# Kernel optimization log

Hardware: AMD Instinct MI355X
Metric: run time of the kernel (lower is better)

## Reference

```python
import math
import jax, jax.numpy as jnp
import numpy as np

LOG2PI = math.log(2.0 * math.pi)
B, T, N, C, K = 16, 12, 325, 64, 8
L = N * T  # 3900, Conv1d in_channels (in_features)


def _l2norm(x, axis):
    # F.normalize(x, dim=axis, p=2) with eps=1e-12
    return x / jnp.maximum(jnp.linalg.norm(x, axis=axis, keepdims=True), 1e-12)


def setup_inputs() -> dict:
    key = jax.random.key(0)
    ks = jax.random.split(key, 5)
    rep = jax.random.normal(ks[0], (B, T, N, C), jnp.float32)
    rep_aug = jax.random.normal(ks[1], (B, T, N, C), jnp.float32)
    # xavier-uniform-scale Linear weight [K, C*N*T]
    W_gamma = jax.random.normal(ks[2], (K, C * N * T), jnp.float32) * 0.005
    # Conv1d(kernel_size=1) weights [K, L]
    W_mu = jax.random.normal(ks[3], (K, L), jnp.float32) * 0.02
    b_mu = jnp.zeros((K,), jnp.float32)
    W_sigma = jax.random.normal(ks[4], (K, L), jnp.float32) * 0.01
    b_sigma = jnp.zeros((K,), jnp.float32)
    return dict(rep=rep, rep_aug=rep_aug, W_gamma=W_gamma, W_mu=W_mu,
                b_mu=b_mu, W_sigma=W_sigma, b_sigma=b_sigma)


def reference(rep, rep_aug, W_gamma, W_mu, b_mu, W_sigma, b_sigma):
    # rep: [b,t,n,c] -> [b,c,n,t]
    rep = jnp.transpose(rep, (0, 3, 2, 1))
    rep_aug = jnp.transpose(rep_aug, (0, 3, 2, 1))
    b, c = rep.shape[0], rep.shape[1]
    rep = _l2norm(rep, 1)
    rep_aug = _l2norm(rep_aug, 1)

    # gammas: softmax(Linear(flat)), [b,k]
    gam = jax.nn.softmax(rep_aug.reshape(b, -1) @ W_gamma.T, axis=-1)

    # Conv1d(kernel=1) on [b, L, c]: out[b,k,j] = sum_l W[k,l]*x[b,l,j] + bias[k]
    xa = jnp.transpose(rep_aug, (0, 2, 3, 1)).reshape(b, -1, c)  # [b,L,c]
    mus = jnp.einsum('kl,blc->bck', W_mu, xa) + b_mu              # [b,c,k]
    sigmas = jnp.exp(jnp.einsum('kl,blc->bck', W_sigma, xa) + b_sigma)

    # log pdf over broadcast [b,c,L,k]
    h = rep.reshape(b, c, -1)                                     # [b,c,L]
    z = (h[:, :, :, None] - mus[:, :, None, :]) / sigmas[:, :, None, :]
    logp = -jnp.log(sigmas)[:, :, None, :] - 0.5 * LOG2PI - 0.5 * z * z

    # prod over channel dim c, then l2norm over L (dim=1 of [b,L,k])
    comp = _l2norm(jnp.prod(logp, axis=1), 1)                     # [b,L,k]
    log_prob = comp + jnp.log(gam)[:, None, :]                    # [b,L,k]
    loss = -jnp.mean(jnp.log(jnp.sum(jnp.exp(log_prob), axis=-1)))
    return loss
```

## Files before the change

### kernel.cpp

```cpp
#include <hip/hip_runtime.h>
#include <hip/hip_bf16.h>
#include <math.h>

#define B_ 16
#define T_ 12
#define N_ 325
#define C_ 64
#define K_ 8
#define L_ 3900
#define M_ 249600
#define M4_ 62400
#define LCH_ 61
#define LOG2PI_ 1.8378770664093453f

#define OFF_LOGGAM 0
#define OFF_PART   128
#define OFF_MUS    384
#define OFF_ISIG   8576
#define OFF_T1     16768
#define OFF_SPART  24960
#define OFF_P      32768
#define OFF_AAUG   531968
#define OFF_GPART  4525568
#define OFF_CONVP  4650368

__global__ __launch_bounds__(256) void kA(const float* __restrict__ rep_aug,
                                          const float* __restrict__ Wmu,
                                          const float* __restrict__ Wsg,
                                          float* __restrict__ Aaug,
                                          float* __restrict__ convp) {
    int b = blockIdx.x / LCH_, lc = blockIdx.x - b * LCH_;
    int l0 = lc * 64;
    __shared__ float ldsA[64 * 65];
    __shared__ float sc[64];
    __shared__ float ldsW[16 * 64];
    int tid = threadIdx.x, lane = tid & 63, wv = tid >> 6;
    const float4* r4 = (const float4*)rep_aug;
    for (int i4 = tid; i4 < 1024; i4 += 256) {
        int ll = i4 >> 4, c4 = i4 & 15;
        int l = l0 + ll;
        float4 v = make_float4(0.f, 0.f, 0.f, 0.f);
        if (l < L_) {
            int n = l / T_, t = l - n * T_;
            v = r4[(size_t)((b * T_ + t) * N_ + n) * 16 + c4];
        }
        int base = ll * 65 + c4 * 4;
        ldsA[base] = v.x; ldsA[base+1] = v.y; ldsA[base+2] = v.z; ldsA[base+3] = v.w;
    }
    for (int idx = tid; idx < 1024; idx += 256) {
        int r = idx >> 6, ll = idx & 63;
        int l = l0 + ll;
        float w = 0.0f;
        if (l < L_) w = (r < 8) ? Wmu[r * L_ + l] : Wsg[(r - 8) * L_ + l];
        ldsW[r * 64 + ll] = w;
    }
    __syncthreads();
    #pragma unroll 4
    for (int i = 0; i < 16; ++i) {
        int p = wv * 16 + i;
        float x = ldsA[p * 65 + lane];
        float ss = x * x;
        #pragma unroll
        for (int m = 1; m < 64; m <<= 1) ss += __shfl_xor(ss, m);
        if (lane == 0) sc[p] = 1.0f / fmaxf(sqrtf(ss), 1e-12f);
    }
    __syncthreads();
    for (int idx = tid; idx < 4096; idx += 256) {
        int c = idx >> 6, ll = idx & 63;
        int l = l0 + ll;
        if (l < L_)
            Aaug[(size_t)(b * C_ + c) * L_ + l] = ldsA[ll * 65 + c] * sc[ll];
    }
    int c = lane, kk = wv;
    const float* w0 = &ldsW[(kk * 4 + 0) * 64];
    const float* w1 = &ldsW[(kk * 4 + 1) * 64];
    const float* w2 = &ldsW[(kk * 4 + 2) * 64];
    const float* w3 = &ldsW[(kk * 4 + 3) * 64];
    float a0 = 0.f, a1 = 0.f, a2 = 0.f, a3 = 0.f;
    #pragma unroll 8
    for (int l = 0; l < 64; ++l) {
        float a = ldsA[l * 65 + c] * sc[l];
        a0 = fmaf(a, w0[l], a0);
        a1 = fmaf(a, w1[l], a1);
        a2 = fmaf(a, w2[l], a2);
        a3 = fmaf(a, w3[l], a3);
    }
    float* dst = convp + (size_t)lc * 16384 + b * 1024 + c * 16 + kk * 4;
    dst[0] = a0; dst[1] = a1; dst[2] = a2; dst[3] = a3;
}

__global__ __launch_bounds__(256) void kB(const float* __restrict__ Aaug,
                                          const float* __restrict__ Wg,
                                          const float* __restrict__ convp,
                                          const float* __restrict__ bmu,
                                          const float* __restrict__ bsg,
                                          float* __restrict__ gpartT,
                                          float* __restrict__ mus,
                                          float* __restrict__ isig,
                                          float* __restrict__ t1) {
    int tid = threadIdx.x, lane = tid & 63, wv = tid >> 6;
    if (blockIdx.x < 975) {
        const float4* A4 = (const float4*)Aaug;
        const float4* W4 = (const float4*)Wg;
        int m4 = blockIdx.x * 64 + lane;
        float4 w[K_];
        #pragma unroll
        for (int k = 0; k < K_; ++k) w[k] = W4[(size_t)k * M4_ + m4];
        float acc[4][K_];
        #pragma unroll
        for (int bb = 0; bb < 4; ++bb) {
            float4 a = A4[(size_t)(wv * 4 + bb) * M4_ + m4];
            #pragma unroll
            for (int k = 0; k < K_; ++k)
                acc[bb][k] = a.x * w[k].x + a.y * w[k].y + a.z * w[k].z + a.w * w[k].w;
        }
        __shared__ float red[128];
        #pragma unroll
        for (int bb = 0; bb < 4; ++bb)
            #pragma unroll
            for (int k = 0; k < K_; ++k) {
                float v = acc[bb][k];
                #pragma unroll
                for (int m = 1; m < 64; m <<= 1) v += __shfl_xor(v, m);
                if (lane == 0) red[wv * 32 + bb * 8 + k] = v;
            }
        __syncthreads();
        if (tid < 128) gpartT[(size_t)tid * 975 + blockIdx.x] = red[tid];
    } else {
        int o = (blockIdx.x - 975) * 256 + tid;
        float s = 0.0f;
        #pragma unroll 8
        for (int lc = 0; lc < LCH_; ++lc) s += convp[(size_t)lc * 16384 + o];
        int bc = o >> 4, kk = o & 15, k = kk & 7;
        if (kk < 8) {
            mus[bc * 8 + k] = s + bmu[k];
        } else {
            float logit = s + bsg[k];
            isig[bc * 8 + k] = expf(-logit);
            t1[bc * 8 + k] = -logit - 0.5f * LOG2PI_;
        }
    }
}

__global__ __launch_bounds__(256) void kC(const float* __restrict__ rep,
                                          const float* __restrict__ gpartT,
                                          const float* __restrict__ mus,
                                          const float* __restrict__ isig,
                                          const float* __restrict__ t1,
                                          float* __restrict__ loggam,
                                          float* __restrict__ P,
                                          float* __restrict__ Spart) {
    int tid = threadIdx.x, lane = tid & 63, wv = tid >> 6;
    if (blockIdx.x < 16) {
        int b = blockIdx.x;
        int k = tid >> 5, i5 = tid & 31;
        float s = 0.0f;
        for (int i = i5; i < 975; i += 32) s += gpartT[(size_t)(b * 8 + k) * 975 + i];
        #pragma unroll
        for (int m = 1; m < 32; m <<= 1) s += __shfl_xor(s, m);
        __shared__ float red[8];
        if (i5 == 0) red[k] = s;
        __syncthreads();
        if (tid < 8) {
            float mx = -1e30f;
            #pragma unroll
            for (int j = 0; j < 8; ++j) mx = fmaxf(mx, red[j]);
            float sum = 0.0f;
            #pragma unroll
            for (int j = 0; j < 8; ++j) sum += expf(red[j] - mx);
            loggam[b * 8 + tid] = red[tid] - mx - logf(sum);
        }
    } else {
        int j = blockIdx.x - 16;
        int b = j / LCH_, lc = j - b * LCH_;
        int l0 = lc * 64;
        __shared__ float ldsA[64 * 65];
        __shared__ float sc[64];
        __shared__ float ldsMu[512], ldsIs[512], ldsT1[512];
        const float4* r4 = (const float4*)rep;
        for (int i4 = tid; i4 < 1024; i4 += 256) {
            int ll = i4 >> 4, c4 = i4 & 15;
            int l = l0 + ll;
            float4 v = make_float4(0.f, 0.f, 0.f, 0.f);
            if (l < L_) {
                int n = l / T_, t = l - n * T_;
                v = r4[(size_t)((b * T_ + t) * N_ + n) * 16 + c4];
            }
            int base = ll * 65 + c4 * 4;
            ldsA[base] = v.x; ldsA[base+1] = v.y; ldsA[base+2] = v.z; ldsA[base+3] = v.w;
        }
        for (int idx = tid; idx < 512; idx += 256) {
            ldsMu[idx] = mus[b * 512 + idx];
            ldsIs[idx] = isig[b * 512 + idx];
            ldsT1[idx] = t1[b * 512 + idx];
        }
        __syncthreads();
        #pragma unroll 4
        for (int i = 0; i < 16; ++i) {
            int p = wv * 16 + i;
            float x = ldsA[p * 65 + lane];
            float ss = x * x;
            #pragma unroll
            for (int m = 1; m < 64; m <<= 1) ss += __shfl_xor(ss, m);
            if (lane == 0) sc[p] = 1.0f / fmaxf(sqrtf(ss), 1e-12f);
        }
        __syncthreads();
        int l = l0 + lane;
        bool valid = l < L_;
        int k0 = wv * 2, k1 = k0 + 1;
        float scv = sc[lane];
        float p0 = 1.0f, p1 = 1.0f;
        #pragma unroll 8
        for (int c = 0; c < 64; ++c) {
            float a = ldsA[lane * 65 + c] * scv;
            float z0 = (a - ldsMu[c * 8 + k0]) * ldsIs[c * 8 + k0];
            p0 *= ldsT1[c * 8 + k0] - 0.5f * z0 * z0;
            float z1 = (a - ldsMu[c * 8 + k1]) * ldsIs[c * 8 + k1];
            p1 *= ldsT1[c * 8 + k1] - 0.5f * z1 * z1;
        }
        if (!valid) { p0 = 0.0f; p1 = 0.0f; }
        if (valid) {
            P[(size_t)(b * K_ + k0) * L_ + l] = p0;
            P[(size_t)(b * K_ + k1) * L_ + l] = p1;
        }
        float v0 = p0 * p0, v1 = p1 * p1;
        #pragma unroll
        for (int m = 1; m < 64; m <<= 1) { v0 += __shfl_xor(v0, m); v1 += __shfl_xor(v1, m); }
        if (lane == 0) {
            Spart[(size_t)(b * K_ + k0) * LCH_ + lc] = v0;
            Spart[(size_t)(b * K_ + k1) * LCH_ + lc] = v1;
        }
    }
}

__global__ __launch_bounds__(256) void kD(const float* __restrict__ P,
                                          const float* __restrict__ Spart,
                                          const float* __restrict__ loggam,
                                          float* __restrict__ part) {
    int b = blockIdx.x >> 4, ch = blockIdx.x & 15;
    int tid = threadIdx.x, lane = tid & 63, wv = tid >> 6;
    __shared__ float invk[8], lgk[8];
    if (tid < 8) {
        float s = 0.0f;
        #pragma unroll 8
        for (int i = 0; i < LCH_; ++i) s += Spart[(size_t)(b * 8 + tid) * LCH_ + i];
        invk[tid] = 1.0f / fmaxf(sqrtf(s), 1e-12f);
        lgk[tid] = loggam[b * 8 + tid];
    }
    __syncthreads();
    int l = ch * 256 + tid;
    float ll = 0.0f;
    if (l < L_) {
        float v[K_];
        float mx = -1e30f;
        #pragma unroll
        for (int k = 0; k < K_; ++k) {
            v[k] = P[(size_t)(b * K_ + k) * L_ + l] * invk[k] + lgk[k];
            mx = fmaxf(mx, v[k]);
        }
        float s = 0.0f;
        #pragma unroll
        for (int k = 0; k < K_; ++k) s += expf(v[k] - mx);
        ll = mx + logf(s);
    }
    #pragma unroll
    for (int m = 1; m < 64; m <<= 1) ll += __shfl_xor(ll, m);
    __shared__ float red[4];
    if (lane == 0) red[wv] = ll;
    __syncthreads();
    if (tid == 0) part[blockIdx.x] = red[0] + red[1] + red[2] + red[3];
}

__global__ void kE(const float* __restrict__ part, float* __restrict__ out) {
    double v = (double)part[threadIdx.x];
    #pragma unroll
    for (int m = 1; m < 64; m <<= 1) v += __shfl_xor(v, m);
    __shared__ double red[4];
    int lane = threadIdx.x & 63, wave = threadIdx.x >> 6;
    if (lane == 0) red[wave] = v;
    __syncthreads();
    if (threadIdx.x == 0)
        out[0] = (float)(-(red[0] + red[1] + red[2] + red[3]) / ((double)B_ * (double)L_));
}

extern "C" void kernel_launch(void* const* d_in, const int* in_sizes, int n_in,
                              void* d_out, int out_size, void* d_ws, size_t ws_size,
                              hipStream_t stream) {
    const float* rep     = (const float*)d_in[0];
    const float* rep_aug = (const float*)d_in[1];
    const float* Wg      = (const float*)d_in[2];
    const float* Wmu     = (const float*)d_in[3];
    const float* bmu     = (const float*)d_in[4];
    const float* Wsg     = (const float*)d_in[5];
    const float* bsg     = (const float*)d_in[6];
    float* out = (float*)d_out;
    float* ws  = (float*)d_ws;

    float* loggam = ws + OFF_LOGGAM;
    float* part   = ws + OFF_PART;
    float* mus    = ws + OFF_MUS;
    float* isig   = ws + OFF_ISIG;
    float* t1     = ws + OFF_T1;
    float* Spart  = ws + OFF_SPART;
    float* P      = ws + OFF_P;
    float* Aaug   = ws + OFF_AAUG;
    float* gpartT = ws + OFF_GPART;
    float* convp  = ws + OFF_CONVP;

    kA<<<B_ * LCH_, 256, 0, stream>>>(rep_aug, Wmu, Wsg, Aaug, convp);
    kB<<<975 + 64, 256, 0, stream>>>(Aaug, Wg, convp, bmu, bsg, gpartT, mus, isig, t1);
    kC<<<16 + B_ * LCH_, 256, 0, stream>>>(rep, gpartT, mus, isig, t1, loggam, P, Spart);
    kD<<<B_ * 16, 256, 0, stream>>>(P, Spart, loggam, part);
    kE<<<1, 256, 0, stream>>>(part, out);
}
```

Measured before the change: 59.72 us.

## Fuse gamma linear into normalization kernel and fold final reduction via atomic counter

The gamma projection (Linear over C*N*T) is now computed inside kA from the normalized rep_aug tile held in LDS. This removes the intermediate Aaug write (about 16 MB) and its reread in kB. Gamma partials per (chunk, batch) are reduced and soft-maxed in a small tail of kB, and the final scalar reduction of kE is merged into kD with a last-block atomic counter, which drops one launch. Block indexing is reordered so batch varies fastest, letting blocks with the same l-chunk share Wg and W loads. The trade-off is that each kA thread now streams Wg rows strided by L, adding global traffic and latency to kA.

```diff
diff --git a/kernel.cpp b/kernel.cpp
--- a/kernel.cpp
+++ b/kernel.cpp
@@ -1,5 +1,4 @@
 #include <hip/hip_runtime.h>
-#include <hip/hip_bf16.h>
 #include <math.h>
 
 #define B_ 16
@@ -9,27 +8,27 @@
 #define K_ 8
 #define L_ 3900
 #define M_ 249600
-#define M4_ 62400
 #define LCH_ 61
 #define LOG2PI_ 1.8378770664093453f
 
 #define OFF_LOGGAM 0
 #define OFF_PART   128
-#define OFF_MUS    384
-#define OFF_ISIG   8576
-#define OFF_T1     16768
-#define OFF_SPART  24960
-#define OFF_P      32768
-#define OFF_AAUG   531968
-#define OFF_GPART  4525568
-#define OFF_CONVP  4650368
+#define OFF_CTR    384
+#define OFF_MUS    512
+#define OFF_ISIG   8704
+#define OFF_T1     16896
+#define OFF_SPART  25088
+#define OFF_GPART  32896
+#define OFF_P      40704
+#define OFF_CONVP  539904
 
 __global__ __launch_bounds__(256) void kA(const float* __restrict__ rep_aug,
+                                          const float* __restrict__ Wg,
                                           const float* __restrict__ Wmu,
                                           const float* __restrict__ Wsg,
-                                          float* __restrict__ Aaug,
+                                          float* __restrict__ gpart,
                                           float* __restrict__ convp) {
-    int b = blockIdx.x / LCH_, lc = blockIdx.x - b * LCH_;
+    int b = blockIdx.x & 15, lc = blockIdx.x >> 4;
     int l0 = lc * 64;
     __shared__ float ldsA[64 * 65];
     __shared__ float sc[64];
@@ -65,69 +64,55 @@
         if (lane == 0) sc[p] = 1.0f / fmaxf(sqrtf(ss), 1e-12f);
     }
     __syncthreads();
-    for (int idx = tid; idx < 4096; idx += 256) {
-        int c = idx >> 6, ll = idx & 63;
-        int l = l0 + ll;
-        if (l < L_)
-            Aaug[(size_t)(b * C_ + c) * L_ + l] = ldsA[ll * 65 + c] * sc[ll];
-    }
     int c = lane, kk = wv;
+    int k0 = wv * 2, k1 = k0 + 1;
     const float* w0 = &ldsW[(kk * 4 + 0) * 64];
     const float* w1 = &ldsW[(kk * 4 + 1) * 64];
     const float* w2 = &ldsW[(kk * 4 + 2) * 64];
     const float* w3 = &ldsW[(kk * 4 + 3) * 64];
+    const float4* wg0 = (const float4*)(Wg + (size_t)k0 * M_ + (size_t)c * L_ + l0);
+    const float4* wg1 = (const float4*)(Wg + (size_t)k1 * M_ + (size_t)c * L_ + l0);
+    int n4 = (L_ - l0 < 64 ? L_ - l0 : 64) >> 2;
     float a0 = 0.f, a1 = 0.f, a2 = 0.f, a3 = 0.f;
-    #pragma unroll 8
-    for (int l = 0; l < 64; ++l) {
-        float a = ldsA[l * 65 + c] * sc[l];
-        a0 = fmaf(a, w0[l], a0);
-        a1 = fmaf(a, w1[l], a1);
-        a2 = fmaf(a, w2[l], a2);
-        a3 = fmaf(a, w3[l], a3);
+    float g0 = 0.f, g1 = 0.f;
+    for (int l4 = 0; l4 < n4; ++l4) {
+        float4 w04 = wg0[l4], w14 = wg1[l4];
+        #pragma unroll
+        for (int j = 0; j < 4; ++j) {
+            int l = l4 * 4 + j;
+            float a = ldsA[l * 65 + c] * sc[l];
+            a0 = fmaf(a, w0[l], a0);
+            a1 = fmaf(a, w1[l], a1);
+            a2 = fmaf(a, w2[l], a2);
+            a3 = fmaf(a, w3[l], a3);
+            float wg0j = j == 0 ? w04.x : j == 1 ? w04.y : j == 2 ? w04.z : w04.w;
+            float wg1j = j == 0 ? w14.x : j == 1 ? w14.y : j == 2 ? w14.z : w14.w;
+            g0 = fmaf(a, wg0j, g0);
+            g1 = fmaf(a, wg1j, g1);
+        }
     }
     float* dst = convp + (size_t)lc * 16384 + b * 1024 + c * 16 + kk * 4;
     dst[0] = a0; dst[1] = a1; dst[2] = a2; dst[3] = a3;
-}
-
-__global__ __launch_bounds__(256) void kB(const float* __restrict__ Aaug,
-                                          const float* __restrict__ Wg,
-                                          const float* __restrict__ convp,
+    #pragma unroll
+    for (int m = 1; m < 64; m <<= 1) { g0 += __shfl_xor(g0, m); g1 += __shfl_xor(g1, m); }
+    if (lane == 0) {
+        gpart[(size_t)blockIdx.x * 8 + k0] = g0;
+        gpart[(size_t)blockIdx.x * 8 + k1] = g1;
+    }
+}
+
+__global__ __launch_bounds__(256) void kB(const float* __restrict__ convp,
+                                          const float* __restrict__ gpart,
                                           const float* __restrict__ bmu,
                                           const float* __restrict__ bsg,
-                                          float* __restrict__ gpartT,
                                           float* __restrict__ mus,
                                           float* __restrict__ isig,
-                                          float* __restrict__ t1) {
-    int tid = threadIdx.x, lane = tid & 63, wv = tid >> 6;
-    if (blockIdx.x < 975) {
-        const float4* A4 = (const float4*)Aaug;
-        const float4* W4 = (const float4*)Wg;
-        int m4 = blockIdx.x * 64 + lane;
-        float4 w[K_];
-        #pragma unroll
-        for (int k = 0; k < K_; ++k) w[k] = W4[(size_t)k * M4_ + m4];
-        float acc[4][K_];
-        #pragma unroll
-        for (int bb = 0; bb < 4; ++bb) {
-            float4 a = A4[(size_t)(wv * 4 + bb) * M4_ + m4];
-            #pragma unroll
-            for (int k = 0; k < K_; ++k)
-                acc[bb][k] = a.x * w[k].x + a.y * w[k].y + a.z * w[k].z + a.w * w[k].w;
-        }
-        __shared__ float red[128];
-        #pragma unroll
-        for (int bb = 0; bb < 4; ++bb)
-            #pragma unroll
-            for (int k = 0; k < K_; ++k) {
-                float v = acc[bb][k];
-                #pragma unroll
-                for (int m = 1; m < 64; m <<= 1) v += __shfl_xor(v, m);
-                if (lane == 0) red[wv * 32 + bb * 8 + k] = v;
-            }
-        __syncthreads();
-        if (tid < 128) gpartT[(size_t)tid * 975 + blockIdx.x] = red[tid];
-    } else {
-        int o = (blockIdx.x - 975) * 256 + tid;
+                                          float* __restrict__ t1,
+                                          float* __restrict__ loggam,
+                                          unsigned* __restrict__ ctr) {
+    int tid = threadIdx.x;
+    if (blockIdx.x < 64) {
+        int o = blockIdx.x * 256 + tid;
         float s = 0.0f;
         #pragma unroll 8
         for (int lc = 0; lc < LCH_; ++lc) s += convp[(size_t)lc * 16384 + o];
@@ -139,104 +124,108 @@
             isig[bc * 8 + k] = expf(-logit);
             t1[bc * 8 + k] = -logit - 0.5f * LOG2PI_;
         }
+    } else {
+        int b = blockIdx.x - 64;
+        if (tid == 0 && b == 0) *ctr = 0u;
+        if (tid < 64) {
+            int lc = tid;
+            bool valid = lc < LCH_;
+            float g[K_];
+            #pragma unroll
+            for (int k = 0; k < K_; ++k)
+                g[k] = valid ? gpart[(size_t)(lc * 16 + b) * 8 + k] : 0.0f;
+            #pragma unroll
+            for (int k = 0; k < K_; ++k)
+                #pragma unroll
+                for (int m = 1; m < 64; m <<= 1) g[k] += __shfl_xor(g[k], m);
+            if (tid == 0) {
+                float mx = -1e30f;
+                #pragma unroll
+                for (int k = 0; k < K_; ++k) mx = fmaxf(mx, g[k]);
+                float sum = 0.0f;
+                #pragma unroll
+                for (int k = 0; k < K_; ++k) sum += expf(g[k] - mx);
+                float lse = mx + logf(sum);
+                #pragma unroll
+                for (int k = 0; k < K_; ++k) loggam[b * 8 + k] = g[k] - lse;
+            }
+        }
     }
 }
 
 __global__ __launch_bounds__(256) void kC(const float* __restrict__ rep,
-                                          const float* __restrict__ gpartT,
                                           const float* __restrict__ mus,
                                           const float* __restrict__ isig,
                                           const float* __restrict__ t1,
-                                          float* __restrict__ loggam,
                                           float* __restrict__ P,
                                           float* __restrict__ Spart) {
+    int b = blockIdx.x & 15, lc = blockIdx.x >> 4;
+    int l0 = lc * 64;
+    __shared__ float ldsA[64 * 65];
+    __shared__ float sc[64];
+    __shared__ float ldsMu[512], ldsIs[512], ldsT1[512];
     int tid = threadIdx.x, lane = tid & 63, wv = tid >> 6;
-    if (blockIdx.x < 16) {
-        int b = blockIdx.x;
-        int k = tid >> 5, i5 = tid & 31;
-        float s = 0.0f;
-        for (int i = i5; i < 975; i += 32) s += gpartT[(size_t)(b * 8 + k) * 975 + i];
-        #pragma unroll
-        for (int m = 1; m < 32; m <<= 1) s += __shfl_xor(s, m);
-        __shared__ float red[8];
-        if (i5 == 0) red[k] = s;
-        __syncthreads();
-        if (tid < 8) {
-            float mx = -1e30f;
-            #pragma unroll
-            for (int j = 0; j < 8; ++j) mx = fmaxf(mx, red[j]);
-            float sum = 0.0f;
-            #pragma unroll
-            for (int j = 0; j < 8; ++j) sum += expf(red[j] - mx);
-            loggam[b * 8 + tid] = red[tid] - mx - logf(sum);
-        }
-    } else {
-        int j = blockIdx.x - 16;
-        int b = j / LCH_, lc = j - b * LCH_;
-        int l0 = lc * 64;
-        __shared__ float ldsA[64 * 65];
-        __shared__ float sc[64];
-        __shared__ float ldsMu[512], ldsIs[512], ldsT1[512];
-        const float4* r4 = (const float4*)rep;
-        for (int i4 = tid; i4 < 1024; i4 += 256) {
-            int ll = i4 >> 4, c4 = i4 & 15;
-            int l = l0 + ll;
-            float4 v = make_float4(0.f, 0.f, 0.f, 0.f);
-            if (l < L_) {
-                int n = l / T_, t = l - n * T_;
-                v = r4[(size_t)((b * T_ + t) * N_ + n) * 16 + c4];
-            }
-            int base = ll * 65 + c4 * 4;
-            ldsA[base] = v.x; ldsA[base+1] = v.y; ldsA[base+2] = v.z; ldsA[base+3] = v.w;
-        }
-        for (int idx = tid; idx < 512; idx += 256) {
-            ldsMu[idx] = mus[b * 512 + idx];
-            ldsIs[idx] = isig[b * 512 + idx];
-            ldsT1[idx] = t1[b * 512 + idx];
-        }
-        __syncthreads();
-        #pragma unroll 4
-        for (int i = 0; i < 16; ++i) {
-            int p = wv * 16 + i;
-            float x = ldsA[p * 65 + lane];
-            float ss = x * x;
-            #pragma unroll
-            for (int m = 1; m < 64; m <<= 1) ss += __shfl_xor(ss, m);
-            if (lane == 0) sc[p] = 1.0f / fmaxf(sqrtf(ss), 1e-12f);
-        }
-        __syncthreads();
-        int l = l0 + lane;
-        bool valid = l < L_;
-        int k0 = wv * 2, k1 = k0 + 1;
-        float scv = sc[lane];
-        float p0 = 1.0f, p1 = 1.0f;
-        #pragma unroll 8
-        for (int c = 0; c < 64; ++c) {
-            float a = ldsA[lane * 65 + c] * scv;
-            float z0 = (a - ldsMu[c * 8 + k0]) * ldsIs[c * 8 + k0];
-            p0 *= ldsT1[c * 8 + k0] - 0.5f * z0 * z0;
-            float z1 = (a - ldsMu[c * 8 + k1]) * ldsIs[c * 8 + k1];
-            p1 *= ldsT1[c * 8 + k1] - 0.5f * z1 * z1;
-        }
-        if (!valid) { p0 = 0.0f; p1 = 0.0f; }
-        if (valid) {
-            P[(size_t)(b * K_ + k0) * L_ + l] = p0;
-            P[(size_t)(b * K_ + k1) * L_ + l] = p1;
-        }
-        float v0 = p0 * p0, v1 = p1 * p1;
-        #pragma unroll
-        for (int m = 1; m < 64; m <<= 1) { v0 += __shfl_xor(v0, m); v1 += __shfl_xor(v1, m); }
-        if (lane == 0) {
-            Spart[(size_t)(b * K_ + k0) * LCH_ + lc] = v0;
-            Spart[(size_t)(b * K_ + k1) * LCH_ + lc] = v1;
-        }
+    const float4* r4 = (const float4*)rep;
+    for (int i4 = tid; i4 < 1024; i4 += 256) {
+        int ll = i4 >> 4, c4 = i4 & 15;
+        int l = l0 + ll;
+        float4 v = make_float4(0.f, 0.f, 0.f, 0.f);
+        if (l < L_) {
+            int n = l / T_, t = l - n * T_;
+            v = r4[(size_t)((b * T_ + t) * N_ + n) * 16 + c4];
+        }
+        int base = ll * 65 + c4 * 4;
+        ldsA[base] = v.x; ldsA[base+1] = v.y; ldsA[base+2] = v.z; ldsA[base+3] = v.w;
+    }
+    for (int idx = tid; idx < 512; idx += 256) {
+        ldsMu[idx] = mus[b * 512 + idx];
+        ldsIs[idx] = isig[b * 512 + idx];
+        ldsT1[idx] = t1[b * 512 + idx];
+    }
+    __syncthreads();
+    #pragma unroll 4
+    for (int i = 0; i < 16; ++i) {
+        int p = wv * 16 + i;
+        float x = ldsA[p * 65 + lane];
+        float ss = x * x;
+        #pragma unroll
+        for (int m = 1; m < 64; m <<= 1) ss += __shfl_xor(ss, m);
+        if (lane == 0) sc[p] = 1.0f / fmaxf(sqrtf(ss), 1e-12f);
+    }
+    __syncthreads();
+    int l = l0 + lane;
+    bool valid = l < L_;
+    int k0 = wv * 2, k1 = k0 + 1;
+    float scv = sc[lane];
+    float p0 = 1.0f, p1 = 1.0f;
+    #pragma unroll 8
+    for (int c = 0; c < 64; ++c) {
+        float a = ldsA[lane * 65 + c] * scv;
+        float z0 = (a - ldsMu[c * 8 + k0]) * ldsIs[c * 8 + k0];
+        p0 *= ldsT1[c * 8 + k0] - 0.5f * z0 * z0;
+        float z1 = (a - ldsMu[c * 8 + k1]) * ldsIs[c * 8 + k1];
+        p1 *= ldsT1[c * 8 + k1] - 0.5f * z1 * z1;
+    }
+    if (!valid) { p0 = 0.0f; p1 = 0.0f; }
+    if (valid) {
+        P[(size_t)(b * K_ + k0) * L_ + l] = p0;
+        P[(size_t)(b * K_ + k1) * L_ + l] = p1;
+    }
+    float v0 = p0 * p0, v1 = p1 * p1;
+    #pragma unroll
+    for (int m = 1; m < 64; m <<= 1) { v0 += __shfl_xor(v0, m); v1 += __shfl_xor(v1, m); }
+    if (lane == 0) {
+        Spart[(size_t)(b * K_ + k0) * LCH_ + lc] = v0;
+        Spart[(size_t)(b * K_ + k1) * LCH_ + lc] = v1;
     }
 }
 
 __global__ __launch_bounds__(256) void kD(const float* __restrict__ P,
                                           const float* __restrict__ Spart,
                                           const float* __restrict__ loggam,
-                                          float* __restrict__ part) {
+                                          float* __restrict__ part,
+                                          unsigned* __restrict__ ctr,
+                                          float* __restrict__ out) {
     int b = blockIdx.x >> 4, ch = blockIdx.x & 15;
     int tid = threadIdx.x, lane = tid & 63, wv = tid >> 6;
     __shared__ float invk[8], lgk[8];
@@ -266,21 +255,28 @@
     #pragma unroll
     for (int m = 1; m < 64; m <<= 1) ll += __shfl_xor(ll, m);
     __shared__ float red[4];
+    __shared__ bool last;
     if (lane == 0) red[wv] = ll;
     __syncthreads();
-    if (tid == 0) part[blockIdx.x] = red[0] + red[1] + red[2] + red[3];
-}
-
-__global__ void kE(const float* __restrict__ part, float* __restrict__ out) {
-    double v = (double)part[threadIdx.x];
-    #pragma unroll
-    for (int m = 1; m < 64; m <<= 1) v += __shfl_xor(v, m);
-    __shared__ double red[4];
-    int lane = threadIdx.x & 63, wave = threadIdx.x >> 6;
-    if (lane == 0) red[wave] = v;
-    __syncthreads();
-    if (threadIdx.x == 0)
-        out[0] = (float)(-(red[0] + red[1] + red[2] + red[3]) / ((double)B_ * (double)L_));
+    if (tid == 0) {
+        float v = red[0] + red[1] + red[2] + red[3];
+        __hip_atomic_store(&part[blockIdx.x], v, __ATOMIC_RELEASE, __HIP_MEMORY_SCOPE_AGENT);
+        unsigned old = __hip_atomic_fetch_add(ctr, 1u, __ATOMIC_ACQ_REL, __HIP_MEMORY_SCOPE_AGENT);
+        last = (old == 255u);
+    }
+    __syncthreads();
+    if (last) {
+        float v = __hip_atomic_load(&part[tid], __ATOMIC_ACQUIRE, __HIP_MEMORY_SCOPE_AGENT);
+        double d = (double)v;
+        #pragma unroll
+        for (int m = 1; m < 64; m <<= 1) d += __shfl_xor(d, m);
+        __shared__ double dred[4];
+        if (lane == 0) dred[wv] = d;
+        __syncthreads();
+        if (tid == 0)
+            out[0] = (float)(-(dred[0] + dred[1] + dred[2] + dred[3]) /
+                             ((double)B_ * (double)L_));
+    }
 }
 
 extern "C" void kernel_launch(void* const* d_in, const int* in_sizes, int n_in,
@@ -296,20 +292,19 @@
     float* out = (float*)d_out;
     float* ws  = (float*)d_ws;
 
-    float* loggam = ws + OFF_LOGGAM;
-    float* part   = ws + OFF_PART;
-    float* mus    = ws + OFF_MUS;
-    float* isig   = ws + OFF_ISIG;
-    float* t1     = ws + OFF_T1;
-    float* Spart  = ws + OFF_SPART;
-    float* P      = ws + OFF_P;
-    float* Aaug   = ws + OFF_AAUG;
-    float* gpartT = ws + OFF_GPART;
-    float* convp  = ws + OFF_CONVP;
-
-    kA<<<B_ * LCH_, 256, 0, stream>>>(rep_aug, Wmu, Wsg, Aaug, convp);
-    kB<<<975 + 64, 256, 0, stream>>>(Aaug, Wg, convp, bmu, bsg, gpartT, mus, isig, t1);
-    kC<<<16 + B_ * LCH_, 256, 0, stream>>>(rep, gpartT, mus, isig, t1, loggam, P, Spart);
-    kD<<<B_ * 16, 256, 0, stream>>>(P, Spart, loggam, part);
-    kE<<<1, 256, 0, stream>>>(part, out);
-}
+    float* loggam  = ws + OFF_LOGGAM;
+    float* part    = ws + OFF_PART;
+    unsigned* ctr  = (unsigned*)(ws + OFF_CTR);
+    float* mus     = ws + OFF_MUS;
+    float* isig    = ws + OFF_ISIG;
+    float* t1      = ws + OFF_T1;
+    float* Spart   = ws + OFF_SPART;
+    float* gpart   = ws + OFF_GPART;
+    float* P       = ws + OFF_P;
+    float* convp   = ws + OFF_CONVP;
+
+    kA<<<B_ * LCH_, 256, 0, stream>>>(rep_aug, Wg, Wmu, Wsg, gpart, convp);
+    kB<<<80, 256, 0, stream>>>(convp, gpart, bmu, bsg, mus, isig, t1, loggam, ctr);
+    kC<<<B_ * LCH_, 256, 0, stream>>>(rep, mus, isig, t1, P, Spart);
+    kD<<<B_ * 16, 256, 0, stream>>>(P, Spart, loggam, part, ctr, out);
+}
```

Result: slower. 76.74 us (+28.5%).

## Fold gamma softmax into kD and replace final kernel with last-block reduction

Applied to the files above, without the earlier changes.

Moves the gamma reduction and log-softmax out of kC into kD, and reorders kC blocks so batch is the fast index. It also drops kE by having the last kD block finish the reduction, using an atomic counter that kB resets. This removes one kernel launch and the loggam round trip. In exchange kD now runs only 16 blocks, each looping over all of L, which cuts parallelism in that stage.

```diff
diff --git a/kernel.cpp b/kernel.cpp
--- a/kernel.cpp
+++ b/kernel.cpp
@@ -1,5 +1,4 @@
 #include <hip/hip_runtime.h>
-#include <hip/hip_bf16.h>
 #include <math.h>
 
 #define B_ 16
@@ -13,16 +12,16 @@
 #define LCH_ 61
 #define LOG2PI_ 1.8378770664093453f
 
-#define OFF_LOGGAM 0
-#define OFF_PART   128
-#define OFF_MUS    384
-#define OFF_ISIG   8576
-#define OFF_T1     16768
-#define OFF_SPART  24960
-#define OFF_P      32768
-#define OFF_AAUG   531968
-#define OFF_GPART  4525568
-#define OFF_CONVP  4650368
+#define OFF_PART   0
+#define OFF_CTR    64
+#define OFF_MUS    128
+#define OFF_ISIG   8320
+#define OFF_T1     16512
+#define OFF_SPART  24704
+#define OFF_GPARTT 32512
+#define OFF_P      157312
+#define OFF_AAUG   656512
+#define OFF_CONVP  4650112
 
 __global__ __launch_bounds__(256) void kA(const float* __restrict__ rep_aug,
                                           const float* __restrict__ Wmu,
@@ -97,7 +96,8 @@
                                           float* __restrict__ gpartT,
                                           float* __restrict__ mus,
                                           float* __restrict__ isig,
-                                          float* __restrict__ t1) {
+                                          float* __restrict__ t1,
+                                          unsigned* __restrict__ ctr) {
     int tid = threadIdx.x, lane = tid & 63, wv = tid >> 6;
     if (blockIdx.x < 975) {
         const float4* A4 = (const float4*)Aaug;
@@ -127,6 +127,7 @@
         __syncthreads();
         if (tid < 128) gpartT[(size_t)tid * 975 + blockIdx.x] = red[tid];
     } else {
+        if (blockIdx.x == 975 && tid == 0) *ctr = 0u;
         int o = (blockIdx.x - 975) * 256 + tid;
         float s = 0.0f;
         #pragma unroll 8
@@ -143,144 +144,151 @@
 }
 
 __global__ __launch_bounds__(256) void kC(const float* __restrict__ rep,
-                                          const float* __restrict__ gpartT,
                                           const float* __restrict__ mus,
                                           const float* __restrict__ isig,
                                           const float* __restrict__ t1,
-                                          float* __restrict__ loggam,
                                           float* __restrict__ P,
                                           float* __restrict__ Spart) {
+    int b = blockIdx.x & 15, lc = blockIdx.x >> 4;
+    int l0 = lc * 64;
+    __shared__ float ldsA[64 * 65];
+    __shared__ float sc[64];
+    __shared__ float ldsMu[512], ldsIs[512], ldsT1[512];
     int tid = threadIdx.x, lane = tid & 63, wv = tid >> 6;
-    if (blockIdx.x < 16) {
-        int b = blockIdx.x;
-        int k = tid >> 5, i5 = tid & 31;
-        float s = 0.0f;
-        for (int i = i5; i < 975; i += 32) s += gpartT[(size_t)(b * 8 + k) * 975 + i];
-        #pragma unroll
-        for (int m = 1; m < 32; m <<= 1) s += __shfl_xor(s, m);
-        __shared__ float red[8];
-        if (i5 == 0) red[k] = s;
-        __syncthreads();
-        if (tid < 8) {
-            float mx = -1e30f;
-            #pragma unroll
-            for (int j = 0; j < 8; ++j) mx = fmaxf(mx, red[j]);
-            float sum = 0.0f;
-            #pragma unroll
-            for (int j = 0; j < 8; ++j) sum += expf(red[j] - mx);
-            loggam[b * 8 + tid] = red[tid] - mx - logf(sum);
-        }
-    } else {
-        int j = blockIdx.x - 16;
-        int b = j / LCH_, lc = j - b * LCH_;
-        int l0 = lc * 64;
-        __shared__ float ldsA[64 * 65];
-        __shared__ float sc[64];
-        __shared__ float ldsMu[512], ldsIs[512], ldsT1[512];
-        const float4* r4 = (const float4*)rep;
-        for (int i4 = tid; i4 < 1024; i4 += 256) {
-            int ll = i4 >> 4, c4 = i4 & 15;
-            int l = l0 + ll;
-            float4 v = make_float4(0.f, 0.f, 0.f, 0.f);
-            if (l < L_) {
-                int n = l / T_, t = l - n * T_;
-                v = r4[(size_t)((b * T_ + t) * N_ + n) * 16 + c4];
-            }
-            int base = ll * 65 + c4 * 4;
-            ldsA[base] = v.x; ldsA[base+1] = v.y; ldsA[base+2] = v.z; ldsA[base+3] = v.w;
-        }
-        for (int idx = tid; idx < 512; idx += 256) {
-            ldsMu[idx] = mus[b * 512 + idx];
-            ldsIs[idx] = isig[b * 512 + idx];
-            ldsT1[idx] = t1[b * 512 + idx];
-        }
-        __syncthreads();
-        #pragma unroll 4
-        for (int i = 0; i < 16; ++i) {
-            int p = wv * 16 + i;
-            float x = ldsA[p * 65 + lane];
-            float ss = x * x;
-            #pragma unroll
-            for (int m = 1; m < 64; m <<= 1) ss += __shfl_xor(ss, m);
-            if (lane == 0) sc[p] = 1.0f / fmaxf(sqrtf(ss), 1e-12f);
-        }
-        __syncthreads();
-        int l = l0 + lane;
-        bool valid = l < L_;
-        int k0 = wv * 2, k1 = k0 + 1;
-        float scv = sc[lane];
-        float p0 = 1.0f, p1 = 1.0f;
-        #pragma unroll 8
-        for (int c = 0; c < 64; ++c) {
-            float a = ldsA[lane * 65 + c] * scv;
-            float z0 = (a - ldsMu[c * 8 + k0]) * ldsIs[c * 8 + k0];
-            p0 *= ldsT1[c * 8 + k0] - 0.5f * z0 * z0;
-            float z1 = (a - ldsMu[c * 8 + k1]) * ldsIs[c * 8 + k1];
-            p1 *= ldsT1[c * 8 + k1] - 0.5f * z1 * z1;
-        }
-        if (!valid) { p0 = 0.0f; p1 = 0.0f; }
-        if (valid) {
-            P[(size_t)(b * K_ + k0) * L_ + l] = p0;
-            P[(size_t)(b * K_ + k1) * L_ + l] = p1;
-        }
-        float v0 = p0 * p0, v1 = p1 * p1;
-        #pragma unroll
-        for (int m = 1; m < 64; m <<= 1) { v0 += __shfl_xor(v0, m); v1 += __shfl_xor(v1, m); }
-        if (lane == 0) {
-            Spart[(size_t)(b * K_ + k0) * LCH_ + lc] = v0;
-            Spart[(size_t)(b * K_ + k1) * LCH_ + lc] = v1;
-        }
+    const float4* r4 = (const float4*)rep;
+    for (int i4 = tid; i4 < 1024; i4 += 256) {
+        int ll = i4 >> 4, c4 = i4 & 15;
+        int l = l0 + ll;
+        float4 v = make_float4(0.f, 0.f, 0.f, 0.f);
+        if (l < L_) {
+            int n = l / T_, t = l - n * T_;
+            v = r4[(size_t)((b * T_ + t) * N_ + n) * 16 + c4];
+        }
+        int base = ll * 65 + c4 * 4;
+        ldsA[base] = v.x; ldsA[base+1] = v.y; ldsA[base+2] = v.z; ldsA[base+3] = v.w;
+    }
+    for (int idx = tid; idx < 512; idx += 256) {
+        ldsMu[idx] = mus[b * 512 + idx];
+        ldsIs[idx] = isig[b * 512 + idx];
+        ldsT1[idx] = t1[b * 512 + idx];
+    }
+    __syncthreads();
+    #pragma unroll 4
+    for (int i = 0; i < 16; ++i) {
+        int p = wv * 16 + i;
+        float x = ldsA[p * 65 + lane];
+        float ss = x * x;
+        #pragma unroll
+        for (int m = 1; m < 64; m <<= 1) ss += __shfl_xor(ss, m);
+        if (lane == 0) sc[p] = 1.0f / fmaxf(sqrtf(ss), 1e-12f);
+    }
+    __syncthreads();
+    int l = l0 + lane;
+    bool valid = l < L_;
+    int k0 = wv * 2, k1i = k0 + 1;
+    float scv = sc[lane];
+    float p0 = 1.0f, p1 = 1.0f;
+    #pragma unroll 8
+    for (int c = 0; c < 64; ++c) {
+        float a = ldsA[lane * 65 + c] * scv;
+        float z0 = (a - ldsMu[c * 8 + k0]) * ldsIs[c * 8 + k0];
+        p0 *= ldsT1[c * 8 + k0] - 0.5f * z0 * z0;
+        float z1 = (a - ldsMu[c * 8 + k1i]) * ldsIs[c * 8 + k1i];
+        p1 *= ldsT1[c * 8 + k1i] - 0.5f * z1 * z1;
+    }
+    if (!valid) { p0 = 0.0f; p1 = 0.0f; }
+    if (valid) {
+        P[(size_t)(b * K_ + k0) * L_ + l] = p0;
+        P[(size_t)(b * K_ + k1i) * L_ + l] = p1;
+    }
+    float v0 = p0 * p0, v1 = p1 * p1;
+    #pragma unroll
+    for (int m = 1; m < 64; m <<= 1) { v0 += __shfl_xor(v0, m); v1 += __shfl_xor(v1, m); }
+    if (lane == 0) {
+        Spart[(size_t)(b * K_ + k0) * LCH_ + lc] = v0;
+        Spart[(size_t)(b * K_ + k1i) * LCH_ + lc] = v1;
     }
 }
 
 __global__ __launch_bounds__(256) void kD(const float* __restrict__ P,
                                           const float* __restrict__ Spart,
-                                          const float* __restrict__ loggam,
-                                          float* __restrict__ part) {
-    int b = blockIdx.x >> 4, ch = blockIdx.x & 15;
+                                          const float* __restrict__ gpartT,
+                                          float* __restrict__ part,
+                                          unsigned* __restrict__ ctr,
+                                          float* __restrict__ out) {
+    int b = blockIdx.x;
     int tid = threadIdx.x, lane = tid & 63, wv = tid >> 6;
-    __shared__ float invk[8], lgk[8];
+    __shared__ float red8[8], lgk[8], invk[8];
+    {
+        int k0 = wv * 2, k1i = k0 + 1;
+        const float* s0 = gpartT + (size_t)(b * 8 + k0) * 975;
+        const float* s1 = gpartT + (size_t)(b * 8 + k1i) * 975;
+        float g0 = 0.f, g1 = 0.f;
+        for (int i = lane; i < 975; i += 64) { g0 += s0[i]; g1 += s1[i]; }
+        #pragma unroll
+        for (int m = 1; m < 64; m <<= 1) { g0 += __shfl_xor(g0, m); g1 += __shfl_xor(g1, m); }
+        if (lane == 0) { red8[k0] = g0; red8[k1i] = g1; }
+    }
+    __syncthreads();
     if (tid < 8) {
         float s = 0.0f;
         #pragma unroll 8
         for (int i = 0; i < LCH_; ++i) s += Spart[(size_t)(b * 8 + tid) * LCH_ + i];
         invk[tid] = 1.0f / fmaxf(sqrtf(s), 1e-12f);
-        lgk[tid] = loggam[b * 8 + tid];
-    }
-    __syncthreads();
-    int l = ch * 256 + tid;
+    } else if (tid == 8) {
+        float mx = -1e30f;
+        #pragma unroll
+        for (int k = 0; k < K_; ++k) mx = fmaxf(mx, red8[k]);
+        float sum = 0.0f;
+        #pragma unroll
+        for (int k = 0; k < K_; ++k) sum += expf(red8[k] - mx);
+        float lse = mx + logf(sum);
+        #pragma unroll
+        for (int k = 0; k < K_; ++k) lgk[k] = red8[k] - lse;
+    }
+    __syncthreads();
+    float ik[K_], lg[K_];
+    #pragma unroll
+    for (int k = 0; k < K_; ++k) { ik[k] = invk[k]; lg[k] = lgk[k]; }
     float ll = 0.0f;
-    if (l < L_) {
-        float v[K_];
-        float mx = -1e30f;
-        #pragma unroll
-        for (int k = 0; k < K_; ++k) {
-            v[k] = P[(size_t)(b * K_ + k) * L_ + l] * invk[k] + lgk[k];
-            mx = fmaxf(mx, v[k]);
-        }
-        float s = 0.0f;
-        #pragma unroll
-        for (int k = 0; k < K_; ++k) s += expf(v[k] - mx);
-        ll = mx + logf(s);
+    for (int i = 0; i < 16; ++i) {
+        int l = i * 256 + tid;
+        if (l < L_) {
+            float v[K_];
+            float mx = -1e30f;
+            #pragma unroll
+            for (int k = 0; k < K_; ++k) {
+                v[k] = P[(size_t)(b * K_ + k) * L_ + l] * ik[k] + lg[k];
+                mx = fmaxf(mx, v[k]);
+            }
+            float s = 0.0f;
+            #pragma unroll
+            for (int k = 0; k < K_; ++k) s += expf(v[k] - mx);
+            ll += mx + logf(s);
+        }
     }
     #pragma unroll
     for (int m = 1; m < 64; m <<= 1) ll += __shfl_xor(ll, m);
     __shared__ float red[4];
+    __shared__ bool last;
     if (lane == 0) red[wv] = ll;
     __syncthreads();
-    if (tid == 0) part[blockIdx.x] = red[0] + red[1] + red[2] + red[3];
-}
-
-__global__ void kE(const float* __restrict__ part, float* __restrict__ out) {
-    double v = (double)part[threadIdx.x];
-    #pragma unroll
-    for (int m = 1; m < 64; m <<= 1) v += __shfl_xor(v, m);
-    __shared__ double red[4];
-    int lane = threadIdx.x & 63, wave = threadIdx.x >> 6;
-    if (lane == 0) red[wave] = v;
-    __syncthreads();
-    if (threadIdx.x == 0)
-        out[0] = (float)(-(red[0] + red[1] + red[2] + red[3]) / ((double)B_ * (double)L_));
+    if (tid == 0) {
+        float v = red[0] + red[1] + red[2] + red[3];
+        __hip_atomic_store(&part[b], v, __ATOMIC_RELEASE, __HIP_MEMORY_SCOPE_AGENT);
+        unsigned old = __hip_atomic_fetch_add(ctr, 1u, __ATOMIC_ACQ_REL,
+                                              __HIP_MEMORY_SCOPE_AGENT);
+        last = (old == (unsigned)(B_ - 1));
+    }
+    __syncthreads();
+    if (last && tid == 0) {
+        double s = 0.0;
+        #pragma unroll
+        for (int b2 = 0; b2 < B_; ++b2)
+            s += (double)__hip_atomic_load(&part[b2], __ATOMIC_ACQUIRE,
+                                           __HIP_MEMORY_SCOPE_AGENT);
+        out[0] = (float)(-s / ((double)B_ * (double)L_));
+    }
 }
 
 extern "C" void kernel_launch(void* const* d_in, const int* in_sizes, int n_in,
@@ -296,20 +304,19 @@
     float* out = (float*)d_out;
     float* ws  = (float*)d_ws;
 
-    float* loggam = ws + OFF_LOGGAM;
-    float* part   = ws + OFF_PART;
-    float* mus    = ws + OFF_MUS;
-    float* isig   = ws + OFF_ISIG;
-    float* t1     = ws + OFF_T1;
-    float* Spart  = ws + OFF_SPART;
-    float* P      = ws + OFF_P;
-    float* Aaug   = ws + OFF_AAUG;
-    float* gpartT = ws + OFF_GPART;
-    float* convp  = ws + OFF_CONVP;
+    float* part    = ws + OFF_PART;
+    unsigned* ctr  = (unsigned*)(ws + OFF_CTR);
+    float* mus     = ws + OFF_MUS;
+    float* isig    = ws + OFF_ISIG;
+    float* t1      = ws + OFF_T1;
+    float* Spart   = ws + OFF_SPART;
+    float* gpartT  = ws + OFF_GPARTT;
+    float* P       = ws + OFF_P;
+    float* Aaug    = ws + OFF_AAUG;
+    float* convp   = ws + OFF_CONVP;
 
     kA<<<B_ * LCH_, 256, 0, stream>>>(rep_aug, Wmu, Wsg, Aaug, convp);
-    kB<<<975 + 64, 256, 0, stream>>>(Aaug, Wg, convp, bmu, bsg, gpartT, mus, isig, t1);
-    kC<<<16 + B_ * LCH_, 256, 0, stream>>>(rep, gpartT, mus, isig, t1, loggam, P, Spart);
-    kD<<<B_ * 16, 256, 0, stream>>>(P, Spart, loggam, part);
-    kE<<<1, 256, 0, stream>>>(part, out);
-}
+    kB<<<975 + 64, 256, 0, stream>>>(Aaug, Wg, convp, bmu, bsg, gpartT, mus, isig, t1, ctr);
+    kC<<<B_ * LCH_, 256, 0, stream>>>(rep, mus, isig, t1, P, Spart);
+    kD<<<B_, 256, 0, stream>>>(P, Spart, gpartT, part, ctr, out);
+}
```

Measured after the change: 79.75 us. 33.5% more time.
